# Performance work log

Measured on AMD Instinct MI355X. Metric: run time of the kernel, lower is better.

## Reference

```python
import jax, jax.numpy as jnp
import numpy as np

C = 64        # channel_n
HID = 128     # hidden_size
HEADS = 4
HD = 16       # head_dim = embed_dim // heads, embed_dim overwritten to channel_n
INNER = HEADS * HD  # 64
MLP = 64
H = W = 64    # img_size
B = 8
STEPS = 6
IN_CH = 1     # input_channels
SCALE = HD ** -0.5


def conv3x3_reflect(x, w, b):
    # x: [B,C,H,W], w: [O,I,3,3] -- reflect padding like nn.Conv2d(padding_mode='reflect')
    xp = jnp.pad(x, ((0, 0), (0, 0), (1, 1), (1, 1)), mode='reflect')
    y = jax.lax.conv_general_dilated(xp, w, (1, 1), 'VALID',
                                     dimension_numbers=('NCHW', 'OIHW', 'NCHW'))
    return y + b[None, :, None, None]


def layernorm(x, w, b, axes):
    mu = jnp.mean(x, axis=axes, keepdims=True)
    var = jnp.var(x, axis=axes, keepdims=True)
    return (x - mu) * jax.lax.rsqrt(var + 1e-5) * w + b


def localize(t, h, w):
    # t: [B,heads,n,d] -> [B,heads,n,9,d]; zero-padded 3x3 neighbourhoods
    # (equivalent to grouped conv with 9 unit-impulse filters, padding='same')
    b, nh, n, d = t.shape
    g = t.reshape(b, nh, h, w, d)
    gp = jnp.pad(g, ((0, 0), (0, 0), (1, 1), (1, 1), (0, 0)))
    nb = jnp.stack([gp[:, :, i:i + h, j:j + w, :]
                    for i in range(3) for j in range(3)], axis=4)
    return nb.reshape(b, nh, n, 9, d)


def attn_block(t, ln_w, ln_b, qkv_w, out_w, out_b):
    y = layernorm(t, ln_w, ln_b, -1)
    qkv = y @ qkv_w.T                              # [B,n,3*inner]
    q, k, v = jnp.split(qkv, 3, axis=-1)
    to_heads = lambda z: z.reshape(z.shape[0], z.shape[1], HEADS, HD).transpose(0, 2, 1, 3)
    q, k, v = to_heads(q), to_heads(k), to_heads(v)   # [B,h,n,d]
    kl = localize(k, H, W)                          # [B,h,n,9,d]
    vl = localize(v, H, W)
    dots = jnp.einsum('bhnd,bhnkd->bhnk', q, kl) * SCALE
    a = jax.nn.softmax(dots, axis=-1)               # [B,h,n,9]
    o = jnp.einsum('bhnk,bhnkd->bhnd', a, vl)
    o = o.transpose(0, 2, 1, 3).reshape(t.shape[0], t.shape[1], INNER)
    return o @ out_w.T + out_b


def ff_block(t, ln_w, ln_b, w1, b1, w2, b2):
    y = layernorm(t, ln_w, ln_b, -1)
    y = jax.nn.gelu(y @ w1.T + b1, approximate=False)
    return y @ w2.T + b2


def setup_inputs() -> dict:
    key = jax.random.key(0)
    ks = jax.random.split(key, 20)
    s = 0.02
    inp = {
        'x': jax.random.normal(ks[0], (B, H, W, C), jnp.float32),
        'masks': jax.random.bernoulli(ks[1], 0.5, (STEPS, B, H, W, 1)),
        'p0_w': jax.random.normal(ks[2], (C, C, 3, 3)) * s,
        'p0_b': jnp.zeros((C,)),
        'p1_w': jax.random.normal(ks[3], (C, C, 3, 3)) * s,
        'p1_b': jnp.zeros((C,)),
        'fc0_w': jax.random.normal(ks[4], (HID, 3 * C)) * s,
        'fc0_b': jnp.zeros((HID,)),
        'fc1_w': jax.random.normal(ks[5], (C, HID)) * s,  # zero-init in torch; random here for a non-trivial test
        'norm0_w': jnp.ones((H, W, HID)),
        'norm0_b': jnp.zeros((H, W, HID)),
        'ln1_w': jnp.ones((C,)),
        'ln1_b': jnp.zeros((C,)),
        'qkv_w': jax.random.normal(ks[6], (3 * INNER, C)) * s,
        'out_w': jax.random.normal(ks[7], (C, INNER)) * s,
        'out_b': jnp.zeros((C,)),
        'ln2_w': jnp.ones((C,)),
        'ln2_b': jnp.zeros((C,)),
        'ff1_w': jax.random.normal(ks[8], (MLP, C)) * s,
        'ff1_b': jnp.zeros((MLP,)),
        'ff2_w': jax.random.normal(ks[9], (C, MLP)) * s,
        'ff2_b': jnp.zeros((C,)),
        'steps': STEPS,
    }
    return inp


def reference(x, masks, p0_w, p0_b, p1_w, p1_b, fc0_w, fc0_b, fc1_w,
              norm0_w, norm0_b, ln1_w, ln1_b, qkv_w, out_w, out_b,
              ln2_w, ln2_b, ff1_w, ff1_b, ff2_w, ff2_b, steps):
    def step(xc, mask):
        # ---- NCA perception + update (BackboneNCA.perceive + fc0/relu/norm/fc1) ----
        xt = xc.transpose(0, 3, 1, 2)                      # [B,C,H,W]
        y1 = conv3x3_reflect(xt, p0_w, p0_b)
        y2 = conv3x3_reflect(xt, p1_w, p1_b)
        p = jnp.concatenate([xt, y1, y2], 1).transpose(0, 2, 3, 1)  # [B,H,W,3C]
        hd = jax.nn.relu(p @ fc0_w.T + fc0_b)              # [B,H,W,HID]
        hd = layernorm(hd, norm0_w, norm0_b, (-3, -2, -1))  # norm0 over [H,W,HID]
        dx = hd @ fc1_w.T                                   # [B,H,W,C]
        dx = dx * mask.astype(xc.dtype)                     # stochastic fire
        xn = xc + dx
        # ---- ViT block with localized (3x3 windowed) attention ----
        t = xn.reshape(B, H * W, C)
        t = t + attn_block(t, ln1_w, ln1_b, qkv_w, out_w, out_b)
        t = t + ff_block(t, ln2_w, ln2_b, ff1_w, ff1_b, ff2_w, ff2_b)
        xn = t.reshape(B, H, W, C)
        # keep input channels unchanged
        xn = jnp.concatenate([xc[..., :IN_CH], xn[..., IN_CH:]], axis=-1)
        return xn, None

    out, _ = jax.lax.scan(step, x, masks)
    return out
```

## Files before the change

### kernel.cpp

```cpp
#include <hip/hip_runtime.h>
#include <hip/hip_bf16.h>

typedef __hip_bfloat16 bf16;
typedef __attribute__((ext_vector_type(8))) short bf16x8;
typedef __attribute__((ext_vector_type(4))) float f32x4;

#define NSTEP 6

static __device__ __forceinline__ float b2f(bf16 v) { return __bfloat162float(v); }

static __device__ __forceinline__ float ldp(const void* p, int i, int md) {
    return md ? ((const float*)p)[i] : b2f(((const bf16*)p)[i]);
}
static __device__ __forceinline__ float finz(float v) {
    return (v == v && v * 0.0f == 0.0f) ? v : 0.0f;
}
static __device__ __forceinline__ unsigned short f2bfu(float v) {
    bf16 h = __float2bfloat16(v);
    return *(unsigned short*)&h;
}

static __device__ __forceinline__ void ld_bf8(const bf16* p, float* f) {
    union { uint4 u; unsigned short s[8]; } r;
    r.u = *(const uint4*)p;
#pragma unroll
    for (int j = 0; j < 8; ++j) f[j] = __uint_as_float(((unsigned)r.s[j]) << 16);
}
static __device__ __forceinline__ void ldp8(const void* p, int i, int md, float* f) {
    if (md) {
        const float* fp = (const float*)p + i;
        float4 a = *(const float4*)fp, b = *(const float4*)(fp + 4);
        f[0]=a.x; f[1]=a.y; f[2]=a.z; f[3]=a.w; f[4]=b.x; f[5]=b.y; f[6]=b.z; f[7]=b.w;
    } else {
        ld_bf8((const bf16*)p + i, f);
    }
}
static __device__ __forceinline__ uint4 pk_bf8(const float* f) {
    union { uint4 u; unsigned short s[8]; } r;
#pragma unroll
    for (int j = 0; j < 8; ++j) r.s[j] = f2bfu(f[j]);
    return r.u;
}


__global__ void k_detect(const uint4* __restrict__ m4,
                         const uint4* __restrict__ x4,
                         int* __restrict__ flags, float* __restrict__ accv) {
    __shared__ int s3f, sup, slo, sf32;
    int t = threadIdx.x;
    if (t == 0) { s3f = 0; sup = 0; slo = 0; sf32 = 0; }
    if (t < 96) accv[t] = 0.f;
    __syncthreads();
    int l3f = 0, lup = 0, llo = 0, lf = 0;
    for (int i = t; i < 3072; i += 256) {
        uint4 v = m4[i];
        const unsigned* d = (const unsigned*)&v;
#pragma unroll
        for (int j = 0; j < 4; ++j) {
            unsigned w = d[j];
            unsigned x3f = w ^ 0x3F3F3F3Fu;
            if ((x3f - 0x01010101u) & ~x3f & 0x80808080u) l3f = 1;
            if (w & 0xFFFFFF00u) lup = 1;
            if (w & 0x0000FFFFu) llo = 1;
        }
    }
    for (int i = t; i < 4096; i += 256) {
        uint4 v = x4[i];
        const unsigned* d = (const unsigned*)&v;
#pragma unroll
        for (int j = 0; j < 4; ++j) {
            unsigned bb = (d[j] >> 8) & 0x7Fu;
            if (bb > 0x48u) lf = 1;
        }
    }
    if (l3f) atomicOr(&s3f, 1);
    if (lup) atomicOr(&sup, 1);
    if (llo) atomicOr(&slo, 1);
    if (lf)  atomicOr(&sf32, 1);
    __syncthreads();
    if (t == 0) {
        int mode;
        if (!s3f && !sup) mode = 0;
        else if (!s3f)    mode = 1;
        else if (slo)     mode = 2;
        else              mode = 3;
        flags[0] = mode;
        flags[1] = sf32;
    }
}

__global__ void k_cast(const void* __restrict__ in, float* __restrict__ out,
                       const int* __restrict__ mflags, int n8) {
    int md = mflags[1];
    int i = blockIdx.x * 256 + threadIdx.x;
    if (i < n8) {
        float f[8];
        ldp8(in, i * 8, md, f);
#pragma unroll
        for (int j = 0; j < 8; ++j) f[j] = finz(f[j]);
        *(float4*)&out[i * 8]     = make_float4(f[0], f[1], f[2], f[3]);
        *(float4*)&out[i * 8 + 4] = make_float4(f[4], f[5], f[6], f[7]);
    }
}

__global__ void k_transpose(const void* __restrict__ in, float* __restrict__ out,
                            const int* __restrict__ mflags, int R, int K) {
    int md = mflags[1];
    int i = blockIdx.x * 256 + threadIdx.x;
    if (i < R * K) {
        int k = i / R, r = i % R;
        out[i] = ldp(in, r * K + k, md);
    }
}

__global__ void k_pack_bf16(const void* __restrict__ in, short* __restrict__ out,
                            const int* __restrict__ mflags, int n) {
    int md = mflags[1];
    int i = blockIdx.x * 256 + threadIdx.x;
    if (i < n) out[i] = (short)f2bfu(ldp(in, i, md));
}

__global__ void k_pack_bt1(const void* __restrict__ p0, const void* __restrict__ p1,
                           short* __restrict__ out, const int* __restrict__ mflags) {
    int md = mflags[1];
    int i = blockIdx.x * 256 + threadIdx.x;
    if (i < 128 * 576) {
        int o = i / 576, k = i % 576;
        int kk = k >> 6, ii = k & 63;
        float v = (o < 64) ? ldp(p0, o * 576 + ii * 9 + kk, md)
                           : ldp(p1, (o - 64) * 576 + ii * 9 + kk, md);
        out[i] = (short)f2bfu(v);
    }
}


__global__ __launch_bounds__(512) void k_perceive(
    const float* __restrict__ xin, const short* __restrict__ bt1,
    const short* __restrict__ fc0s, const void* __restrict__ p0b,
    const void* __restrict__ p1b, const void* __restrict__ fc0b,
    const int* __restrict__ mflags, bf16* __restrict__ hd,
    float* __restrict__ accv, int step)
{
    __shared__ __align__(16) short xpad_s[3 * 66 * 72];
    __shared__ __align__(16) short P_s[64 * 200];
    __shared__ float red[32];
    int md = mflags[1];
    int bh = blockIdx.x;
    int b = bh >> 6, h = bh & 63;
    int t = threadIdx.x;

    for (int e = t; e < 1536; e += 512) {
        int c8 = e & 7, w = (e >> 3) & 63, r = e >> 9;
        int hr = h - 1 + r; hr = hr < 0 ? -hr : (hr > 63 ? 126 - hr : hr);
        const float* src = xin + ((((b << 6) + hr) << 6) | w) * 64 + c8 * 8;
        float f[8];
        float4 v0 = *(const float4*)src, v1 = *(const float4*)(src + 4);
        f[0]=v0.x; f[1]=v0.y; f[2]=v0.z; f[3]=v0.w; f[4]=v1.x; f[5]=v1.y; f[6]=v1.z; f[7]=v1.w;
        uint4 pv = pk_bf8(f);
        *(uint4*)&xpad_s[((r * 66) + w + 1) * 72 + c8 * 8] = pv;
        if (r == 1) *(uint4*)&P_s[w * 200 + c8 * 8] = pv;
    }
    if (t < 48) {
        int c8 = t & 7, side = (t >> 3) & 1, r = t >> 4;
        int hr = h - 1 + r; hr = hr < 0 ? -hr : (hr > 63 ? 126 - hr : hr);
        int wsrc = side ? 62 : 1, wp = side ? 65 : 0;
        const float* src = xin + ((((b << 6) + hr) << 6) | wsrc) * 64 + c8 * 8;
        float f[8];
        float4 v0 = *(const float4*)src, v1 = *(const float4*)(src + 4);
        f[0]=v0.x; f[1]=v0.y; f[2]=v0.z; f[3]=v0.w; f[4]=v1.x; f[5]=v1.y; f[6]=v1.z; f[7]=v1.w;
        *(uint4*)&xpad_s[((r * 66) + wp) * 72 + c8 * 8] = pk_bf8(f);
    }
    __syncthreads();

    int og  = __builtin_amdgcn_readfirstlane(t >> 6);
    int l   = t & 63, nl = l & 15, q = l >> 4;
    int mt0 = (og & 1) * 2;
    int nt0 = (og >> 1) * 2;
    int o0  = nt0 * 16 + nl, o1 = o0 + 16;

    f32x4 acc[2][2];
#pragma unroll
    for (int i = 0; i < 2; ++i)
#pragma unroll
        for (int j = 0; j < 2; ++j) acc[i][j] = (f32x4){0.f, 0.f, 0.f, 0.f};

    for (int kt = 0; kt < 18; ++kt) {
        int kk = kt >> 1, c0 = (kt & 1) << 5;
        int r = kk / 3, cxi = kk - r * 3;
        bf16x8 b0 = *(const bf16x8*)(bt1 + o0 * 576 + kt * 32 + q * 8);
        bf16x8 b1 = *(const bf16x8*)(bt1 + o1 * 576 + kt * 32 + q * 8);
        bf16x8 a0 = *(const bf16x8*)&xpad_s[((r * 66) + mt0 * 16 + nl + cxi) * 72 + c0 + q * 8];
        bf16x8 a1 = *(const bf16x8*)&xpad_s[((r * 66) + mt0 * 16 + 16 + nl + cxi) * 72 + c0 + q * 8];
        acc[0][0] = __builtin_amdgcn_mfma_f32_16x16x32_bf16(a0, b0, acc[0][0], 0, 0, 0);
        acc[0][1] = __builtin_amdgcn_mfma_f32_16x16x32_bf16(a0, b1, acc[0][1], 0, 0, 0);
        acc[1][0] = __builtin_amdgcn_mfma_f32_16x16x32_bf16(a1, b0, acc[1][0], 0, 0, 0);
        acc[1][1] = __builtin_amdgcn_mfma_f32_16x16x32_bf16(a1, b1, acc[1][1], 0, 0, 0);
    }
    {
        float bias0 = (o0 < 64) ? ldp(p0b, o0, md) : ldp(p1b, o0 - 64, md);
        float bias1 = (o1 < 64) ? ldp(p0b, o1, md) : ldp(p1b, o1 - 64, md);
#pragma unroll
        for (int i = 0; i < 2; ++i)
#pragma unroll
            for (int j = 0; j < 2; ++j) {
                int oo = j ? o1 : o0;
                float bb = j ? bias1 : bias0;
#pragma unroll
                for (int r2 = 0; r2 < 4; ++r2) {
                    int m = (mt0 + i) * 16 + q * 4 + r2;
                    P_s[m * 200 + 64 + oo] = (short)f2bfu(acc[i][j][r2] + bb);
                }
            }
    }
    __syncthreads();

#pragma unroll
    for (int i = 0; i < 2; ++i)
#pragma unroll
        for (int j = 0; j < 2; ++j) acc[i][j] = (f32x4){0.f, 0.f, 0.f, 0.f};
    for (int kt = 0; kt < 6; ++kt) {
        bf16x8 b0 = *(const bf16x8*)(fc0s + o0 * 192 + kt * 32 + q * 8);
        bf16x8 b1 = *(const bf16x8*)(fc0s + o1 * 192 + kt * 32 + q * 8);
        bf16x8 a0 = *(const bf16x8*)&P_s[(mt0 * 16 + nl) * 200 + kt * 32 + q * 8];
        bf16x8 a1 = *(const bf16x8*)&P_s[(mt0 * 16 + 16 + nl) * 200 + kt * 32 + q * 8];
        acc[0][0] = __builtin_amdgcn_mfma_f32_16x16x32_bf16(a0, b0, acc[0][0], 0, 0, 0);
        acc[0][1] = __builtin_amdgcn_mfma_f32_16x16x32_bf16(a0, b1, acc[0][1], 0, 0, 0);
        acc[1][0] = __builtin_amdgcn_mfma_f32_16x16x32_bf16(a1, b0, acc[1][0], 0, 0, 0);
        acc[1][1] = __builtin_amdgcn_mfma_f32_16x16x32_bf16(a1, b1, acc[1][1], 0, 0, 0);
    }
    float lsum = 0.f, lsq = 0.f;
    {
        float fb0 = ldp(fc0b, o0, md), fb1 = ldp(fc0b, o1, md);
#pragma unroll
        for (int i = 0; i < 2; ++i)
#pragma unroll
            for (int j = 0; j < 2; ++j) {
                int oo = j ? o1 : o0;
                float bb = j ? fb1 : fb0;
#pragma unroll
                for (int r2 = 0; r2 < 4; ++r2) {
                    int m = (mt0 + i) * 16 + q * 4 + r2;
                    float v = fmaxf(acc[i][j][r2] + bb, 0.f);
                    unsigned short hu = f2bfu(v);
                    hd[((bh << 6) + m) * 128 + oo] = *(bf16*)&hu;
                    float vr = __uint_as_float(((unsigned)hu) << 16);
                    lsum += vr; lsq += vr * vr;
                }
            }
    }
#pragma unroll
    for (int off = 32; off > 0; off >>= 1) {
        lsum += __shfl_down(lsum, off, 64);
        lsq  += __shfl_down(lsq,  off, 64);
    }
    if (l == 0) { red[og] = lsum; red[16 + og] = lsq; }
    __syncthreads();
    if (t == 0) {
        float a = 0.f, s2 = 0.f;
#pragma unroll
        for (int w = 0; w < 8; ++w) { a += red[w]; s2 += red[16 + w]; }
        atomicAdd(&accv[step * 16 + b * 2],     a);
        atomicAdd(&accv[step * 16 + b * 2 + 1], s2);
    }
}

__global__ __launch_bounds__(512) void k_update_qkv(
    float* __restrict__ xio, const bf16* __restrict__ hd,
    const float* __restrict__ fc1t, const void* __restrict__ n0w,
    const void* __restrict__ n0b, const void* __restrict__ mraw,
    const int* __restrict__ mflags, const float* __restrict__ accv,
    float* __restrict__ c0buf, const float* __restrict__ qkvt,
    const void* __restrict__ ln1w, const void* __restrict__ ln1b,
    bf16* __restrict__ qkv, int step)
{
    __shared__ float hdn[64 * 129];
    __shared__ float ys[64 * 65];
    int md = mflags[1];
    int bh = blockIdx.x;
    int b = bh >> 6, h = bh & 63;
    int t = threadIdx.x;
    const float invN = 1.f / 524288.f;
    float mean = accv[step * 16 + b * 2] * invN;
    float var  = accv[step * 16 + b * 2 + 1] * invN - mean * mean;
    float rstd = rsqrtf(fmaxf(var, 0.f) + 1e-5f);

    const bf16* hrow = hd + ((b * 64 + h) * 64) * 128;
    for (int e = t; e < 1024; e += 512) {
        int pos = e >> 4, j8 = (e & 15) * 8;
        float hv[8], wv[8], bv[8];
        ld_bf8(hrow + pos * 128 + j8, hv);
        int ni = (h * 64 + pos) * 128 + j8;
        ldp8(n0w, ni, md, wv);
        ldp8(n0b, ni, md, bv);
#pragma unroll
        for (int j = 0; j < 8; ++j)
            hdn[pos * 129 + j8 + j] = (hv[j] - mean) * rstd * wv[j] + bv[j];
    }
    __syncthreads();

    int cg  = __builtin_amdgcn_readfirstlane(t >> 6);
    int pos = t & 63;
    float acc[8];
#pragma unroll
    for (int ci = 0; ci < 8; ++ci) acc[ci] = 0.f;
    for (int j = 0; j < 128; ++j) {
        float hv = hdn[pos * 129 + j];
        const float* fw = fc1t + j * 64 + cg * 8;
#pragma unroll
        for (int ci = 0; ci < 8; ++ci) acc[ci] = fmaf(fw[ci], hv, acc[ci]);
    }
    int mmode = mflags[0];
    int midx = ((step * 8 + b) * 64 + h) * 64 + pos;
    int m;
    if (mmode == 0)      m = ((const int*)mraw)[midx] != 0;
    else if (mmode == 1) m = ((const unsigned char*)mraw)[midx] != 0;
    else if (mmode == 2) m = ((const unsigned short*)mraw)[midx] != 0;
    else                 m = ((const float*)mraw)[midx] != 0.0f;

    int idx = ((b * 64 + h) * 64 + pos) * 64 + cg * 8;
    float4 x0 = *(const float4*)&xio[idx];
    float4 x1 = *(const float4*)&xio[idx + 4];
    float xv[8] = {x0.x, x0.y, x0.z, x0.w, x1.x, x1.y, x1.z, x1.w};
    if (cg == 0) c0buf[(b * 64 + h) * 64 + pos] = xv[0];
    float xn[8];
#pragma unroll
    for (int ci = 0; ci < 8; ++ci) {
        xn[ci] = finz(m ? (xv[ci] + acc[ci]) : xv[ci]);
        ys[pos * 65 + cg * 8 + ci] = xn[ci];
    }
    *(float4*)&xio[idx]     = make_float4(xn[0], xn[1], xn[2], xn[3]);
    *(float4*)&xio[idx + 4] = make_float4(xn[4], xn[5], xn[6], xn[7]);
    __syncthreads();

    {
        int tok = t >> 3, j8 = (t & 7) * 8;
        float v[8];
        float ls = 0.f, lq = 0.f;
#pragma unroll
        for (int ci = 0; ci < 8; ++ci) {
            v[ci] = ys[tok * 65 + j8 + ci];
            ls += v[ci]; lq += v[ci] * v[ci];
        }
#pragma unroll
        for (int off = 1; off < 8; off <<= 1) {
            ls += __shfl_xor(ls, off, 64);
            lq += __shfl_xor(lq, off, 64);
        }
        float mu = ls * (1.f / 64.f);
        float vr = lq * (1.f / 64.f) - mu * mu;
        float rs = rsqrtf(fmaxf(vr, 0.f) + 1e-5f);
        float wv[8], bv[8];
        ldp8(ln1w, j8, md, wv);
        ldp8(ln1b, j8, md, bv);
#pragma unroll
        for (int ci = 0; ci < 8; ++ci)
            ys[tok * 65 + j8 + ci] = (v[ci] - mu) * rs * wv[ci] + bv[ci];
    }
    __syncthreads();

    float a2[24];
#pragma unroll
    for (int oi = 0; oi < 24; ++oi) a2[oi] = 0.f;
    for (int c = 0; c < 64; ++c) {
        float yv = ys[pos * 65 + c];
        const float* qw = qkvt + c * 192 + cg * 24;
#pragma unroll
        for (int oi = 0; oi < 24; ++oi) a2[oi] = fmaf(qw[oi], yv, a2[oi]);
    }
    union { uint4 u[3]; unsigned short s[24]; } pq;
#pragma unroll
    for (int oi = 0; oi < 24; ++oi) pq.s[oi] = f2bfu(a2[oi]);
    uint4* qrow = (uint4*)(qkv + (((b * 64 + h) * 64) + pos) * 192 + cg * 24);
    qrow[0] = pq.u[0]; qrow[1] = pq.u[1]; qrow[2] = pq.u[2];
}

__global__ __launch_bounds__(512) void k_attn_ff(
    const bf16* __restrict__ qkv, float* __restrict__ xio,
    const float* __restrict__ c0buf, const short* __restrict__ outs,
    const short* __restrict__ ff1s, const short* __restrict__ ff2s,
    const void* __restrict__ outb, const void* __restrict__ ln2w,
    const void* __restrict__ ln2b, const void* __restrict__ ff1b,
    const void* __restrict__ ff2b, const int* __restrict__ mflags,
    void* __restrict__ dout, int write_out)
{
    __shared__ __align__(16) char smraw[50944];
    float* kv = (float*)smraw;
    short* Ao = (short*)smraw;
    float* ts = (float*)(smraw + 9216);
    short* ys = (short*)(smraw + 25856);
    short* hs = (short*)(smraw + 35072);

    int md = mflags[1];
    int bh = blockIdx.x;
    int b = bh >> 6, h = bh & 63;
    int t = threadIdx.x;

    if (t < 192) {
        int c = t & 63, r = t >> 6;
        kv[c * 199 + r * 66]      = 0.f;
        kv[c * 199 + r * 66 + 65] = 0.f;
    }
    for (int e = t; e < 1536; e += 512) {
        int c8 = (e & 7) * 8, w = (e >> 3) & 63, r = e >> 9;
        int hr = h - 1 + r;
        float f[8];
        if (hr >= 0 && hr <= 63) {
            ld_bf8(qkv + ((b * 64 + hr) * 64 + w) * 192 + 64 + c8, f);
        } else {
#pragma unroll
            for (int j = 0; j < 8; ++j) f[j] = 0.f;
        }
#pragma unroll
        for (int j = 0; j < 8; ++j) kv[(c8 + j) * 199 + r * 66 + w + 1] = f[j];
    }
    __syncthreads();

    int head = __builtin_amdgcn_readfirstlane((t >> 6) & 3);
    int pos  = t & 63;
    float q[16];
    {
        const bf16* qr = qkv + (((b * 64 + h) * 64) + pos) * 192 + head * 16;
        ld_bf8(qr, q); ld_bf8(qr + 8, q + 8);
    }

    float a[9];
#pragma unroll
    for (int r = 0; r < 3; ++r)
#pragma unroll
        for (int cxi = 0; cxi < 3; ++cxi) {
            float dot = 0.f;
#pragma unroll
            for (int d = 0; d < 16; ++d)
                dot = fmaf(q[d], kv[(head * 16 + d) * 199 + r * 66 + pos + cxi], dot);
            a[r * 3 + cxi] = dot * 0.25f;
        }
    float mx = a[0];
#pragma unroll
    for (int k = 1; k < 9; ++k) mx = fmaxf(mx, a[k]);
    float ssum = 0.f;
#pragma unroll
    for (int k = 0; k < 9; ++k) { a[k] = __expf(a[k] - mx); ssum += a[k]; }
    float inv = 1.f / ssum;
#pragma unroll
    for (int k = 0; k < 9; ++k) a[k] *= inv;
    __syncthreads();

    for (int e = t; e < 1536; e += 512) {
        int c8 = (e & 7) * 8, w = (e >> 3) & 63, r = e >> 9;
        int hr = h - 1 + r;
        float f[8];
        if (hr >= 0 && hr <= 63) {
            ld_bf8(qkv + ((b * 64 + hr) * 64 + w) * 192 + 128 + c8, f);
        } else {
#pragma unroll
            for (int j = 0; j < 8; ++j) f[j] = 0.f;
        }
#pragma unroll
        for (int j = 0; j < 8; ++j) kv[(c8 + j) * 199 + r * 66 + w + 1] = f[j];
    }
    __syncthreads();

    float o[16];
#pragma unroll
    for (int d = 0; d < 16; ++d) {
        float ov = 0.f;
#pragma unroll
        for (int r = 0; r < 3; ++r)
#pragma unroll
            for (int cxi = 0; cxi < 3; ++cxi)
                ov = fmaf(a[r * 3 + cxi], kv[(head * 16 + d) * 199 + r * 66 + pos + cxi], ov);
        o[d] = ov;
    }
    __syncthreads();

    if (t < 256) {
        *(uint4*)&Ao[pos * 72 + head * 16]     = pk_bf8(o);
        *(uint4*)&Ao[pos * 72 + head * 16 + 8] = pk_bf8(o + 8);
    }
    __syncthreads();

    int og = __builtin_amdgcn_readfirstlane(t >> 6);
    int l = t & 63, nl = l & 15, qd = l >> 4;
    int mt = og & 3;
    int nt0 = (og >> 2) * 2;
    int o0 = nt0 * 16 + nl, o1 = o0 + 16;

    {
        f32x4 pa[2];
        pa[0] = (f32x4){0.f,0.f,0.f,0.f}; pa[1] = (f32x4){0.f,0.f,0.f,0.f};
#pragma unroll
        for (int kt = 0; kt < 2; ++kt) {
            bf16x8 av = *(const bf16x8*)&Ao[(mt * 16 + nl) * 72 + kt * 32 + qd * 8];
            bf16x8 b0 = *(const bf16x8*)(outs + o0 * 64 + kt * 32 + qd * 8);
            bf16x8 b1 = *(const bf16x8*)(outs + o1 * 64 + kt * 32 + qd * 8);
            pa[0] = __builtin_amdgcn_mfma_f32_16x16x32_bf16(av, b0, pa[0], 0, 0, 0);
            pa[1] = __builtin_amdgcn_mfma_f32_16x16x32_bf16(av, b1, pa[1], 0, 0, 0);
        }
        float ob0 = ldp(outb, o0, md), ob1 = ldp(outb, o1, md);
#pragma unroll
        for (int j = 0; j < 2; ++j)
#pragma unroll
            for (int r2 = 0; r2 < 4; ++r2) {
                int m = mt * 16 + qd * 4 + r2;
                ts[m * 65 + (j ? o1 : o0)] = pa[j][r2] + (j ? ob1 : ob0);
            }
    }
    __syncthreads();

    int idx = ((bh << 6) + pos) * 64 + (t >> 6) * 8;
    {
        int cg2 = t >> 6;
        float4 x0 = *(const float4*)&xio[idx];
        float4 x1 = *(const float4*)&xio[idx + 4];
        float* tp = &ts[pos * 65 + cg2 * 8];
        tp[0] += x0.x; tp[1] += x0.y; tp[2] += x0.z; tp[3] += x0.w;
        tp[4] += x1.x; tp[5] += x1.y; tp[6] += x1.z; tp[7] += x1.w;
    }
    __syncthreads();

    {
        int tok = t >> 3, j8 = (t & 7) * 8;
        float v[8];
        float ls = 0.f, lq = 0.f;
#pragma unroll
        for (int ci = 0; ci < 8; ++ci) {
            v[ci] = ts[tok * 65 + j8 + ci];
            ls += v[ci]; lq += v[ci] * v[ci];
        }
#pragma unroll
        for (int off = 1; off < 8; off <<= 1) {
            ls += __shfl_xor(ls, off, 64);
            lq += __shfl_xor(lq, off, 64);
        }
        float mu = ls * (1.f / 64.f);
        float vr = lq * (1.f / 64.f) - mu * mu;
        float rs = rsqrtf(fmaxf(vr, 0.f) + 1e-5f);
        float wv[8], bv[8];
        ldp8(ln2w, j8, md, wv);
        ldp8(ln2b, j8, md, bv);
        float yv[8];
#pragma unroll
        for (int ci = 0; ci < 8; ++ci) yv[ci] = (v[ci] - mu) * rs * wv[ci] + bv[ci];
        *(uint4*)&ys[tok * 72 + j8] = pk_bf8(yv);
    }
    __syncthreads();

    {
        f32x4 ma[2];
        ma[0] = (f32x4){0.f,0.f,0.f,0.f}; ma[1] = (f32x4){0.f,0.f,0.f,0.f};
#pragma unroll
        for (int kt = 0; kt < 2; ++kt) {
            bf16x8 av = *(const bf16x8*)&ys[(mt * 16 + nl) * 72 + kt * 32 + qd * 8];
            bf16x8 b0 = *(const bf16x8*)(ff1s + o0 * 64 + kt * 32 + qd * 8);
            bf16x8 b1 = *(const bf16x8*)(ff1s + o1 * 64 + kt * 32 + qd * 8);
            ma[0] = __builtin_amdgcn_mfma_f32_16x16x32_bf16(av, b0, ma[0], 0, 0, 0);
            ma[1] = __builtin_amdgcn_mfma_f32_16x16x32_bf16(av, b1, ma[1], 0, 0, 0);
        }
        float f1b0 = ldp(ff1b, o0, md), f1b1 = ldp(ff1b, o1, md);
#pragma unroll
        for (int j = 0; j < 2; ++j)
#pragma unroll
            for (int r2 = 0; r2 < 4; ++r2) {
                int m = mt * 16 + qd * 4 + r2;
                float v = ma[j][r2] + (j ? f1b1 : f1b0);
                float g = 0.5f * v * (1.f + erff(v * 0.70710678118654752f));
                hs[m * 72 + (j ? o1 : o0)] = (short)f2bfu(g);
            }
    }
    __syncthreads();

    {
        f32x4 fa[2];
        fa[0] = (f32x4){0.f,0.f,0.f,0.f}; fa[1] = (f32x4){0.f,0.f,0.f,0.f};
#pragma unroll
        for (int kt = 0; kt < 2; ++kt) {
            bf16x8 av = *(const bf16x8*)&hs[(mt * 16 + nl) * 72 + kt * 32 + qd * 8];
            bf16x8 b0 = *(const bf16x8*)(ff2s + o0 * 64 + kt * 32 + qd * 8);
            bf16x8 b1 = *(const bf16x8*)(ff2s + o1 * 64 + kt * 32 + qd * 8);
            fa[0] = __builtin_amdgcn_mfma_f32_16x16x32_bf16(av, b0, fa[0], 0, 0, 0);
            fa[1] = __builtin_amdgcn_mfma_f32_16x16x32_bf16(av, b1, fa[1], 0, 0, 0);
        }
        float f2b0 = ldp(ff2b, o0, md), f2b1 = ldp(ff2b, o1, md);
#pragma unroll
        for (int j = 0; j < 2; ++j)
#pragma unroll
            for (int r2 = 0; r2 < 4; ++r2) {
                int m = mt * 16 + qd * 4 + r2;
                int oo = j ? o1 : o0;
                ts[m * 65 + oo] += fa[j][r2] + (j ? f2b1 : f2b0);
            }
    }
    __syncthreads();

    {
        int cg2 = t >> 6;
        float fv[8];
#pragma unroll
        for (int ci = 0; ci < 8; ++ci) {
            float v = ts[pos * 65 + cg2 * 8 + ci];
            if (cg2 == 0 && ci == 0) v = c0buf[(bh << 6) + pos];
            fv[ci] = finz(v);
        }
        *(float4*)&xio[idx]     = make_float4(fv[0], fv[1], fv[2], fv[3]);
        *(float4*)&xio[idx + 4] = make_float4(fv[4], fv[5], fv[6], fv[7]);
        if (write_out) {
            if (md) {
                *(float4*)&((float*)dout)[idx]     = make_float4(fv[0], fv[1], fv[2], fv[3]);
                *(float4*)&((float*)dout)[idx + 4] = make_float4(fv[4], fv[5], fv[6], fv[7]);
            } else {
                *(uint4*)&((bf16*)dout)[idx] = pk_bf8(fv);
            }
        }
    }
}


extern "C" void kernel_launch(void* const* d_in, const int* in_sizes, int n_in,
                              void* d_out, int out_size, void* d_ws, size_t ws_size,
                              hipStream_t stream) {
    (void)in_sizes; (void)n_in; (void)out_size; (void)ws_size;
    const void* x     = d_in[0];
    const void* masks = d_in[1];
    const void* p0w   = d_in[2];
    const void* p0b   = d_in[3];
    const void* p1w   = d_in[4];
    const void* p1b   = d_in[5];
    const void* fc0w  = d_in[6];
    const void* fc0b  = d_in[7];
    const void* fc1w  = d_in[8];
    const void* n0w   = d_in[9];
    const void* n0b   = d_in[10];
    const void* ln1w  = d_in[11];
    const void* ln1b  = d_in[12];
    const void* qkvw  = d_in[13];
    const void* outw  = d_in[14];
    const void* outb  = d_in[15];
    const void* ln2w  = d_in[16];
    const void* ln2b  = d_in[17];
    const void* ff1w  = d_in[18];
    const void* ff1b  = d_in[19];
    const void* ff2w  = d_in[20];
    const void* ff2b  = d_in[21];

    char* wsb = (char*)d_ws;
    float* xst    = (float*)(wsb + 0);
    bf16*  hd     = (bf16*) (wsb + 8388608);
    bf16*  qkvb   = (bf16*) (wsb + 8388608);
    float* c0buf  = (float*)(wsb + 20971520);
    short* bt1    = (short*)(wsb + 21102592);
    short* fc0s   = (short*)(wsb + 21397504);
    float* fc1t   = (float*)(wsb + 21446656);
    float* qkvt   = (float*)(wsb + 21479424);
    short* outs   = (short*)(wsb + 21528576);
    short* ff1s   = (short*)(wsb + 21536768);
    short* ff2s   = (short*)(wsb + 21544960);
    float* accv   = (float*)(wsb + 21553152);
    int*   mflags = (int*)  (wsb + 21553536);

    k_detect<<<1, 256, 0, stream>>>((const uint4*)masks, (const uint4*)x, mflags, accv);
    k_cast<<<1024, 256, 0, stream>>>(x, xst, mflags, 262144);
    k_pack_bt1<<<288, 256, 0, stream>>>(p0w, p1w, bt1, mflags);
    k_pack_bf16<<<96, 256, 0, stream>>>(fc0w, fc0s, mflags, 24576);
    k_transpose<<<32, 256, 0, stream>>>(fc1w, fc1t, mflags, 64, 128);
    k_transpose<<<48, 256, 0, stream>>>(qkvw, qkvt, mflags, 192, 64);
    k_pack_bf16<<<16, 256, 0, stream>>>(outw, outs, mflags, 4096);
    k_pack_bf16<<<16, 256, 0, stream>>>(ff1w, ff1s, mflags, 4096);
    k_pack_bf16<<<16, 256, 0, stream>>>(ff2w, ff2s, mflags, 4096);

    for (int s = 0; s < NSTEP; ++s) {
        k_perceive<<<512, 512, 0, stream>>>(xst, bt1, fc0s, p0b, p1b, fc0b, mflags, hd, accv, s);
        k_update_qkv<<<512, 512, 0, stream>>>(xst, hd, fc1t, n0w, n0b, masks, mflags, accv,
                                              c0buf, qkvt, ln1w, ln1b, qkvb, s);
        k_attn_ff<<<512, 512, 0, stream>>>(qkvb, xst, c0buf, outs, ff1s, ff2s,
                                           outb, ln2w, ln2b, ff1b, ff2b, mflags,
                                           d_out, (s == NSTEP - 1) ? 1 : 0);
    }
}
```

Baseline: 705.0 us.

## Use MFMA for fc1 and QKV projections, stage K/V together in bf16 LDS

```diff
diff --git a/kernel.cpp b/kernel.cpp
--- a/kernel.cpp
+++ b/kernel.cpp
@@ -103,21 +103,21 @@
     }
 }
 
-__global__ void k_transpose(const void* __restrict__ in, float* __restrict__ out,
-                            const int* __restrict__ mflags, int R, int K) {
+__global__ void k_pack_multi(const void* __restrict__ pa, const void* __restrict__ pb,
+                             const void* __restrict__ pc, const void* __restrict__ pd,
+                             const void* __restrict__ pe, const void* __restrict__ pf,
+                             short* __restrict__ out, const int* __restrict__ mflags) {
     int md = mflags[1];
     int i = blockIdx.x * 256 + threadIdx.x;
-    if (i < R * K) {
-        int k = i / R, r = i % R;
-        out[i] = ldp(in, r * K + k, md);
-    }
-}
-
-__global__ void k_pack_bf16(const void* __restrict__ in, short* __restrict__ out,
-                            const int* __restrict__ mflags, int n) {
-    int md = mflags[1];
-    int i = blockIdx.x * 256 + threadIdx.x;
-    if (i < n) out[i] = (short)f2bfu(ldp(in, i, md));
+    if (i >= 57344) return;
+    float v;
+    if      (i < 24576) v = ldp(pa, i, md);
+    else if (i < 32768) v = ldp(pb, i - 24576, md);
+    else if (i < 45056) v = ldp(pc, i - 32768, md);
+    else if (i < 49152) v = ldp(pd, i - 45056, md);
+    else if (i < 53248) v = ldp(pe, i - 49152, md);
+    else                v = ldp(pf, i - 53248, md);
+    out[i] = (short)f2bfu(v);
 }
 
 __global__ void k_pack_bt1(const void* __restrict__ p0, const void* __restrict__ p1,
@@ -266,15 +266,19 @@
 
 __global__ __launch_bounds__(512) void k_update_qkv(
     float* __restrict__ xio, const bf16* __restrict__ hd,
-    const float* __restrict__ fc1t, const void* __restrict__ n0w,
+    const short* __restrict__ fc1s, const void* __restrict__ n0w,
     const void* __restrict__ n0b, const void* __restrict__ mraw,
     const int* __restrict__ mflags, const float* __restrict__ accv,
-    float* __restrict__ c0buf, const float* __restrict__ qkvt,
+    float* __restrict__ c0buf, const short* __restrict__ qkvs,
     const void* __restrict__ ln1w, const void* __restrict__ ln1b,
     bf16* __restrict__ qkv, int step)
 {
-    __shared__ float hdn[64 * 129];
-    __shared__ float ys[64 * 65];
+    __shared__ __align__(16) char sm[43264];
+    short* hdn = (short*)sm;
+    float* ts  = (float*)(sm + 17408);
+    short* ys  = (short*)(sm + 34048);
+    short* qo  = (short*)sm;
+
     int md = mflags[1];
     int bh = blockIdx.x;
     int b = bh >> 6, h = bh & 63;
@@ -287,49 +291,67 @@
     const bf16* hrow = hd + ((b * 64 + h) * 64) * 128;
     for (int e = t; e < 1024; e += 512) {
         int pos = e >> 4, j8 = (e & 15) * 8;
-        float hv[8], wv[8], bv[8];
+        float hv[8], wv[8], bv[8], f[8];
         ld_bf8(hrow + pos * 128 + j8, hv);
         int ni = (h * 64 + pos) * 128 + j8;
         ldp8(n0w, ni, md, wv);
         ldp8(n0b, ni, md, bv);
 #pragma unroll
-        for (int j = 0; j < 8; ++j)
-            hdn[pos * 129 + j8 + j] = (hv[j] - mean) * rstd * wv[j] + bv[j];
-    }
-    __syncthreads();
-
-    int cg  = __builtin_amdgcn_readfirstlane(t >> 6);
+        for (int j = 0; j < 8; ++j) f[j] = (hv[j] - mean) * rstd * wv[j] + bv[j];
+        *(uint4*)&hdn[pos * 136 + j8] = pk_bf8(f);
+    }
+    __syncthreads();
+
+    int og = __builtin_amdgcn_readfirstlane(t >> 6);
+    int l = t & 63, nl = l & 15, q = l >> 4;
+
+    {
+        int mt = og & 3, nh = og >> 2;
+        int o0 = nh * 32 + nl, o1 = o0 + 16;
+        f32x4 a0 = (f32x4){0.f,0.f,0.f,0.f}, a1 = (f32x4){0.f,0.f,0.f,0.f};
+#pragma unroll
+        for (int kt = 0; kt < 4; ++kt) {
+            bf16x8 av = *(const bf16x8*)&hdn[(mt * 16 + nl) * 136 + kt * 32 + q * 8];
+            bf16x8 b0 = *(const bf16x8*)(fc1s + o0 * 128 + kt * 32 + q * 8);
+            bf16x8 b1 = *(const bf16x8*)(fc1s + o1 * 128 + kt * 32 + q * 8);
+            a0 = __builtin_amdgcn_mfma_f32_16x16x32_bf16(av, b0, a0, 0, 0, 0);
+            a1 = __builtin_amdgcn_mfma_f32_16x16x32_bf16(av, b1, a1, 0, 0, 0);
+        }
+#pragma unroll
+        for (int r2 = 0; r2 < 4; ++r2) {
+            int m = mt * 16 + q * 4 + r2;
+            ts[m * 65 + o0] = a0[r2];
+            ts[m * 65 + o1] = a1[r2];
+        }
+    }
+    __syncthreads();
+
+    int cg = og;
     int pos = t & 63;
-    float acc[8];
-#pragma unroll
-    for (int ci = 0; ci < 8; ++ci) acc[ci] = 0.f;
-    for (int j = 0; j < 128; ++j) {
-        float hv = hdn[pos * 129 + j];
-        const float* fw = fc1t + j * 64 + cg * 8;
-#pragma unroll
-        for (int ci = 0; ci < 8; ++ci) acc[ci] = fmaf(fw[ci], hv, acc[ci]);
-    }
-    int mmode = mflags[0];
-    int midx = ((step * 8 + b) * 64 + h) * 64 + pos;
-    int m;
-    if (mmode == 0)      m = ((const int*)mraw)[midx] != 0;
-    else if (mmode == 1) m = ((const unsigned char*)mraw)[midx] != 0;
-    else if (mmode == 2) m = ((const unsigned short*)mraw)[midx] != 0;
-    else                 m = ((const float*)mraw)[midx] != 0.0f;
-
-    int idx = ((b * 64 + h) * 64 + pos) * 64 + cg * 8;
-    float4 x0 = *(const float4*)&xio[idx];
-    float4 x1 = *(const float4*)&xio[idx + 4];
-    float xv[8] = {x0.x, x0.y, x0.z, x0.w, x1.x, x1.y, x1.z, x1.w};
-    if (cg == 0) c0buf[(b * 64 + h) * 64 + pos] = xv[0];
-    float xn[8];
-#pragma unroll
-    for (int ci = 0; ci < 8; ++ci) {
-        xn[ci] = finz(m ? (xv[ci] + acc[ci]) : xv[ci]);
-        ys[pos * 65 + cg * 8 + ci] = xn[ci];
-    }
-    *(float4*)&xio[idx]     = make_float4(xn[0], xn[1], xn[2], xn[3]);
-    *(float4*)&xio[idx + 4] = make_float4(xn[4], xn[5], xn[6], xn[7]);
+    {
+        int mmode = mflags[0];
+        int midx = ((step * 8 + b) * 64 + h) * 64 + pos;
+        int mk;
+        if (mmode == 0)      mk = ((const int*)mraw)[midx] != 0;
+        else if (mmode == 1) mk = ((const unsigned char*)mraw)[midx] != 0;
+        else if (mmode == 2) mk = ((const unsigned short*)mraw)[midx] != 0;
+        else                 mk = ((const float*)mraw)[midx] != 0.0f;
+
+        int idx = ((b * 64 + h) * 64 + pos) * 64 + cg * 8;
+        float4 x0 = *(const float4*)&xio[idx];
+        float4 x1 = *(const float4*)&xio[idx + 4];
+        float xv[8] = {x0.x, x0.y, x0.z, x0.w, x1.x, x1.y, x1.z, x1.w};
+        if (cg == 0) c0buf[(b * 64 + h) * 64 + pos] = xv[0];
+        float* tp = &ts[pos * 65 + cg * 8];
+        float xn[8];
+#pragma unroll
+        for (int ci = 0; ci < 8; ++ci) {
+            xn[ci] = finz(mk ? (xv[ci] + tp[ci]) : xv[ci]);
+            tp[ci] = xn[ci];
+        }
+        *(float4*)&xio[idx]     = make_float4(xn[0], xn[1], xn[2], xn[3]);
+        *(float4*)&xio[idx + 4] = make_float4(xn[4], xn[5], xn[6], xn[7]);
+    }
     __syncthreads();
 
     {
@@ -338,7 +360,7 @@
         float ls = 0.f, lq = 0.f;
 #pragma unroll
         for (int ci = 0; ci < 8; ++ci) {
-            v[ci] = ys[tok * 65 + j8 + ci];
+            v[ci] = ts[tok * 65 + j8 + ci];
             ls += v[ci]; lq += v[ci] * v[ci];
         }
 #pragma unroll
@@ -352,26 +374,42 @@
         float wv[8], bv[8];
         ldp8(ln1w, j8, md, wv);
         ldp8(ln1b, j8, md, bv);
-#pragma unroll
-        for (int ci = 0; ci < 8; ++ci)
-            ys[tok * 65 + j8 + ci] = (v[ci] - mu) * rs * wv[ci] + bv[ci];
-    }
-    __syncthreads();
-
-    float a2[24];
-#pragma unroll
-    for (int oi = 0; oi < 24; ++oi) a2[oi] = 0.f;
-    for (int c = 0; c < 64; ++c) {
-        float yv = ys[pos * 65 + c];
-        const float* qw = qkvt + c * 192 + cg * 24;
-#pragma unroll
-        for (int oi = 0; oi < 24; ++oi) a2[oi] = fmaf(qw[oi], yv, a2[oi]);
-    }
-    union { uint4 u[3]; unsigned short s[24]; } pq;
-#pragma unroll
-    for (int oi = 0; oi < 24; ++oi) pq.s[oi] = f2bfu(a2[oi]);
-    uint4* qrow = (uint4*)(qkv + (((b * 64 + h) * 64) + pos) * 192 + cg * 24);
-    qrow[0] = pq.u[0]; qrow[1] = pq.u[1]; qrow[2] = pq.u[2];
+        float yv[8];
+#pragma unroll
+        for (int ci = 0; ci < 8; ++ci) yv[ci] = (v[ci] - mu) * rs * wv[ci] + bv[ci];
+        *(uint4*)&ys[tok * 72 + j8] = pk_bf8(yv);
+    }
+    __syncthreads();
+
+    {
+        int mt = og & 3, nh = og >> 2;
+        f32x4 qa[6];
+#pragma unroll
+        for (int n = 0; n < 6; ++n) qa[n] = (f32x4){0.f, 0.f, 0.f, 0.f};
+#pragma unroll
+        for (int kt = 0; kt < 2; ++kt) {
+            bf16x8 av = *(const bf16x8*)&ys[(mt * 16 + nl) * 72 + kt * 32 + q * 8];
+#pragma unroll
+            for (int n = 0; n < 6; ++n) {
+                bf16x8 bv = *(const bf16x8*)(qkvs + (((nh * 6 + n) * 16) + nl) * 64 + kt * 32 + q * 8);
+                qa[n] = __builtin_amdgcn_mfma_f32_16x16x32_bf16(av, bv, qa[n], 0, 0, 0);
+            }
+        }
+#pragma unroll
+        for (int n = 0; n < 6; ++n)
+#pragma unroll
+            for (int r2 = 0; r2 < 4; ++r2) {
+                int m = mt * 16 + q * 4 + r2;
+                qo[m * 200 + (nh * 6 + n) * 16 + nl] = (short)f2bfu(qa[n][r2]);
+            }
+    }
+    __syncthreads();
+
+    for (int e = t; e < 1536; e += 512) {
+        int p2 = e / 24, c8 = e - p2 * 24;
+        *(uint4*)(qkv + ((bh << 6) + p2) * 192 + c8 * 8) =
+            *(const uint4*)&qo[p2 * 200 + c8 * 8];
+    }
 }
 
 __global__ __launch_bounds__(512) void k_attn_ff(
@@ -383,8 +421,9 @@
     const void* __restrict__ ff2b, const int* __restrict__ mflags,
     void* __restrict__ dout, int write_out)
 {
-    __shared__ __align__(16) char smraw[50944];
-    float* kv = (float*)smraw;
+    __shared__ __align__(16) char smraw[57024];
+    short* Ks = (short*)smraw;
+    short* Vs = (short*)(smraw + 28512);
     short* Ao = (short*)smraw;
     float* ts = (float*)(smraw + 9216);
     short* ys = (short*)(smraw + 25856);
@@ -395,85 +434,75 @@
     int b = bh >> 6, h = bh & 63;
     int t = threadIdx.x;
 
-    if (t < 192) {
-        int c = t & 63, r = t >> 6;
-        kv[c * 199 + r * 66]      = 0.f;
-        kv[c * 199 + r * 66 + 65] = 0.f;
-    }
-    for (int e = t; e < 1536; e += 512) {
-        int c8 = (e & 7) * 8, w = (e >> 3) & 63, r = e >> 9;
+    if (t < 96) {
+        int kind = (t >= 48) ? 1 : 0, u = t - kind * 48;
+        int r = u >> 4, side = (u >> 3) & 1, c8 = u & 7;
+        short* dst = kind ? Vs : Ks;
+        uint4 z = {0, 0, 0, 0};
+        *(uint4*)&dst[((r * 66) + (side ? 65 : 0)) * 72 + c8 * 8] = z;
+    }
+    for (int e = t; e < 3072; e += 512) {
+        int kind = (e >= 1536) ? 1 : 0, u = e - kind * 1536;
+        int c8 = u & 7, w = (u >> 3) & 63, r = u >> 9;
         int hr = h - 1 + r;
-        float f[8];
-        if (hr >= 0 && hr <= 63) {
-            ld_bf8(qkv + ((b * 64 + hr) * 64 + w) * 192 + 64 + c8, f);
-        } else {
-#pragma unroll
-            for (int j = 0; j < 8; ++j) f[j] = 0.f;
-        }
-#pragma unroll
-        for (int j = 0; j < 8; ++j) kv[(c8 + j) * 199 + r * 66 + w + 1] = f[j];
-    }
-    __syncthreads();
-
-    int head = __builtin_amdgcn_readfirstlane((t >> 6) & 3);
+        uint4 v = {0, 0, 0, 0};
+        if (hr >= 0 && hr <= 63)
+            v = *(const uint4*)(qkv + ((b * 64 + hr) * 64 + w) * 192 + 64 + kind * 64 + c8 * 8);
+        short* dst = kind ? Vs : Ks;
+        *(uint4*)&dst[((r * 66) + w + 1) * 72 + c8 * 8] = v;
+    }
+    __syncthreads();
+
+    int head = __builtin_amdgcn_readfirstlane(t >> 6) & 3;
     int pos  = t & 63;
-    float q[16];
-    {
+    bool act = t < 256;
+    float o[16];
+    if (act) {
+        float qv[16];
         const bf16* qr = qkv + (((b * 64 + h) * 64) + pos) * 192 + head * 16;
-        ld_bf8(qr, q); ld_bf8(qr + 8, q + 8);
-    }
-
-    float a[9];
-#pragma unroll
-    for (int r = 0; r < 3; ++r)
-#pragma unroll
-        for (int cxi = 0; cxi < 3; ++cxi) {
-            float dot = 0.f;
-#pragma unroll
-            for (int d = 0; d < 16; ++d)
-                dot = fmaf(q[d], kv[(head * 16 + d) * 199 + r * 66 + pos + cxi], dot);
-            a[r * 3 + cxi] = dot * 0.25f;
-        }
-    float mx = a[0];
-#pragma unroll
-    for (int k = 1; k < 9; ++k) mx = fmaxf(mx, a[k]);
-    float ssum = 0.f;
-#pragma unroll
-    for (int k = 0; k < 9; ++k) { a[k] = __expf(a[k] - mx); ssum += a[k]; }
-    float inv = 1.f / ssum;
-#pragma unroll
-    for (int k = 0; k < 9; ++k) a[k] *= inv;
-    __syncthreads();
-
-    for (int e = t; e < 1536; e += 512) {
-        int c8 = (e & 7) * 8, w = (e >> 3) & 63, r = e >> 9;
-        int hr = h - 1 + r;
-        float f[8];
-        if (hr >= 0 && hr <= 63) {
-            ld_bf8(qkv + ((b * 64 + hr) * 64 + w) * 192 + 128 + c8, f);
-        } else {
-#pragma unroll
-            for (int j = 0; j < 8; ++j) f[j] = 0.f;
-        }
-#pragma unroll
-        for (int j = 0; j < 8; ++j) kv[(c8 + j) * 199 + r * 66 + w + 1] = f[j];
-    }
-    __syncthreads();
-
-    float o[16];
-#pragma unroll
-    for (int d = 0; d < 16; ++d) {
-        float ov = 0.f;
+        ld_bf8(qr, qv); ld_bf8(qr + 8, qv + 8);
+
+        float a9[9];
 #pragma unroll
         for (int r = 0; r < 3; ++r)
 #pragma unroll
-            for (int cxi = 0; cxi < 3; ++cxi)
-                ov = fmaf(a[r * 3 + cxi], kv[(head * 16 + d) * 199 + r * 66 + pos + cxi], ov);
-        o[d] = ov;
-    }
-    __syncthreads();
-
-    if (t < 256) {
+            for (int cxi = 0; cxi < 3; ++cxi) {
+                const short* kp = &Ks[((r * 66) + pos + cxi) * 72 + head * 16];
+                float kf[16];
+                ld_bf8((const bf16*)kp, kf);
+                ld_bf8((const bf16*)(kp + 8), kf + 8);
+                float dot = 0.f;
+#pragma unroll
+                for (int d = 0; d < 16; ++d) dot = fmaf(qv[d], kf[d], dot);
+                a9[r * 3 + cxi] = dot * 0.25f;
+            }
+        float mx = a9[0];
+#pragma unroll
+        for (int k = 1; k < 9; ++k) mx = fmaxf(mx, a9[k]);
+        float ssum = 0.f;
+#pragma unroll
+        for (int k = 0; k < 9; ++k) { a9[k] = __expf(a9[k] - mx); ssum += a9[k]; }
+        float inv = 1.f / ssum;
+#pragma unroll
+        for (int k = 0; k < 9; ++k) a9[k] *= inv;
+
+#pragma unroll
+        for (int d = 0; d < 16; ++d) o[d] = 0.f;
+#pragma unroll
+        for (int r = 0; r < 3; ++r)
+#pragma unroll
+            for (int cxi = 0; cxi < 3; ++cxi) {
+                const short* vp = &Vs[((r * 66) + pos + cxi) * 72 + head * 16];
+                float vf[16];
+                ld_bf8((const bf16*)vp, vf);
+                ld_bf8((const bf16*)(vp + 8), vf + 8);
+                float w = a9[r * 3 + cxi];
+#pragma unroll
+                for (int d = 0; d < 16; ++d) o[d] = fmaf(w, vf[d], o[d]);
+            }
+    }
+    __syncthreads();
+    if (act) {
         *(uint4*)&Ao[pos * 72 + head * 16]     = pk_bf8(o);
         *(uint4*)&Ao[pos * 72 + head * 16 + 8] = pk_bf8(o + 8);
     }
@@ -645,32 +674,29 @@
     char* wsb = (char*)d_ws;
     float* xst    = (float*)(wsb + 0);
     bf16*  hd     = (bf16*) (wsb + 8388608);
-    bf16*  qkvb   = (bf16*) (wsb + 8388608);
-    float* c0buf  = (float*)(wsb + 20971520);
-    short* bt1    = (short*)(wsb + 21102592);
-    short* fc0s   = (short*)(wsb + 21397504);
-    float* fc1t   = (float*)(wsb + 21446656);
-    float* qkvt   = (float*)(wsb + 21479424);
-    short* outs   = (short*)(wsb + 21528576);
-    short* ff1s   = (short*)(wsb + 21536768);
-    short* ff2s   = (short*)(wsb + 21544960);
-    float* accv   = (float*)(wsb + 21553152);
-    int*   mflags = (int*)  (wsb + 21553536);
+    bf16*  qkvb   = (bf16*) (wsb + 16777216);
+    float* c0buf  = (float*)(wsb + 29360128);
+    short* bt1    = (short*)(wsb + 29491200);
+    short* packs  = (short*)(wsb + 29638656);
+    float* accv   = (float*)(wsb + 29753344);
+    int*   mflags = (int*)  (wsb + 29753728);
+
+    short* fc0s = packs;
+    short* fc1s = packs + 24576;
+    short* qkvs = packs + 32768;
+    short* outs = packs + 45056;
+    short* ff1s = packs + 49152;
+    short* ff2s = packs + 53248;
 
     k_detect<<<1, 256, 0, stream>>>((const uint4*)masks, (const uint4*)x, mflags, accv);
     k_cast<<<1024, 256, 0, stream>>>(x, xst, mflags, 262144);
     k_pack_bt1<<<288, 256, 0, stream>>>(p0w, p1w, bt1, mflags);
-    k_pack_bf16<<<96, 256, 0, stream>>>(fc0w, fc0s, mflags, 24576);
-    k_transpose<<<32, 256, 0, stream>>>(fc1w, fc1t, mflags, 64, 128);
-    k_transpose<<<48, 256, 0, stream>>>(qkvw, qkvt, mflags, 192, 64);
-    k_pack_bf16<<<16, 256, 0, stream>>>(outw, outs, mflags, 4096);
-    k_pack_bf16<<<16, 256, 0, stream>>>(ff1w, ff1s, mflags, 4096);
-    k_pack_bf16<<<16, 256, 0, stream>>>(ff2w, ff2s, mflags, 4096);
+    k_pack_multi<<<224, 256, 0, stream>>>(fc0w, fc1w, qkvw, outw, ff1w, ff2w, packs, mflags);
 
     for (int s = 0; s < NSTEP; ++s) {
         k_perceive<<<512, 512, 0, stream>>>(xst, bt1, fc0s, p0b, p1b, fc0b, mflags, hd, accv, s);
-        k_update_qkv<<<512, 512, 0, stream>>>(xst, hd, fc1t, n0w, n0b, masks, mflags, accv,
-                                              c0buf, qkvt, ln1w, ln1b, qkvb, s);
+        k_update_qkv<<<512, 512, 0, stream>>>(xst, hd, fc1s, n0w, n0b, masks, mflags, accv,
+                                              c0buf, qkvs, ln1w, ln1b, qkvb, s);
         k_attn_ff<<<512, 512, 0, stream>>>(qkvb, xst, c0buf, outs, ff1s, ff2s,
                                            outb, ln2w, ln2b, ff1b, ff2b, mflags,
                                            d_out, (s == NSTEP - 1) ? 1 : 0);
```

New measurement: 592.9 us. -15.9%, faster.
